# Kernel optimization log

Hardware: AMD Instinct MI355X
Metric: run time of the kernel (lower is better)

The kernel has to match this reference:

```python
import math
import jax, jax.numpy as jnp
import numpy as np

B, T, C = 2, 2048, 1024
N_HEAD = 16
HEAD_DIM = C // N_HEAD

def setup_inputs() -> dict:
    key = jax.random.key(0)
    kx, kq, kk, kv, kp = jax.random.split(key, 5)
    s = 1.0 / math.sqrt(C)
    return {
        "x": jax.random.normal(kx, (B, T, C), dtype=jnp.float32),
        "Wq": jax.random.normal(kq, (C, C), dtype=jnp.float32) * s,
        "Wk": jax.random.normal(kk, (C, C), dtype=jnp.float32) * s,
        "Wv": jax.random.normal(kv, (C, C), dtype=jnp.float32) * s,
        "Wproj": jax.random.normal(kp, (C, C), dtype=jnp.float32) * s,
    }

def reference(x, Wq, Wk, Wv, Wproj):
    b, t, c = x.shape
    # nn.Linear(no bias): x @ W.T ; weights stored [out, in]
    def heads(w):
        return (x @ w.T).reshape(b, t, N_HEAD, HEAD_DIM).transpose(0, 2, 1, 3)  # [B,H,T,D]
    q, k, v = heads(Wq), heads(Wk), heads(Wv)
    att = jnp.einsum('bhqd,bhkd->bhqk', q, k) / math.sqrt(HEAD_DIM)  # [B,H,T,T]
    causal = jnp.tril(jnp.ones((t, t), dtype=bool))
    att = jnp.where(causal, att, -jnp.inf)
    att = jax.nn.softmax(att, axis=-1)
    y = jnp.einsum('bhqk,bhkd->bhqd', att, v)           # [B,H,T,D]
    y = y.transpose(0, 2, 1, 3).reshape(b, t, c)        # [B,T,C]
    return y @ Wproj.T
```

## Files before the change

kernel.cpp:

```cpp
#include <hip/hip_runtime.h>
#include <stdint.h>

typedef uint16_t u16;
typedef uint32_t u32;
typedef __attribute__((ext_vector_type(8))) _Float16 f16x8;
typedef __attribute__((ext_vector_type(4))) float f32x4;

#define NB 2
#define NT 2048
#define NC 1024
#define NH 16
#define ND 64
#define NM (NB*NT)
#define LOG2E 1.44269504088896340736f

__device__ __forceinline__ u16 f2h(float f) {
  _Float16 h = (_Float16)f;
  return __builtin_bit_cast(u16, h);
}

__global__ __launch_bounds__(256) void cvt_kernel(const float* __restrict__ src,
                                                  u16* __restrict__ dst, int n4) {
  int i = blockIdx.x * 256 + threadIdx.x;
  if (i >= n4) return;
  float4 v = ((const float4*)src)[i];
  ushort4 o;
  o.x = f2h(v.x); o.y = f2h(v.y); o.z = f2h(v.z); o.w = f2h(v.w);
  ((ushort4*)dst)[i] = o;
}

__global__ __launch_bounds__(256) void cvtw_kernel(const float* __restrict__ w0,
                                                   const float* __restrict__ w1,
                                                   const float* __restrict__ w2,
                                                   const float* __restrict__ w3,
                                                   u16* __restrict__ dst) {
  int i = blockIdx.x * 256 + threadIdx.x;
  int which = i >> 18;
  const float* src = (which == 0) ? w0 : (which == 1) ? w1 : (which == 2) ? w2 : w3;
  int j = i & 262143;
  float4 v = ((const float4*)src)[j];
  ushort4 o;
  o.x = f2h(v.x); o.y = f2h(v.y); o.z = f2h(v.z); o.w = f2h(v.w);
  ((ushort4*)dst)[i] = o;
}

__device__ __forceinline__ void gload16(const void* g, void* l) {
  __builtin_amdgcn_global_load_lds(
      (const __attribute__((address_space(1))) void*)g,
      (__attribute__((address_space(3))) void*)l, 16, 0, 0);
}

template<int EPI>
__global__ __launch_bounds__(256) void gemm_bt(const u16* __restrict__ A,
                                               const u16* __restrict__ Bw,
                                               int K, int N,
                                               u16* __restrict__ oq, u16* __restrict__ okk,
                                               u16* __restrict__ ovt,
                                               float* __restrict__ of) {
  __shared__ __align__(16) u16 SH[4*128*64];
  u16* Al = SH;
  u16* Bl = SH + 2*128*64;
  const int tid = threadIdx.x, lane = tid & 63, wid = tid >> 6;
  const int g = lane >> 4, qq = lane & 15;
  const int wm = wid >> 1, wn = wid & 1;
  const int m0 = blockIdx.y * 128, n0 = blockIdx.x * 128;
  const int srow = lane >> 3;
  const int scol8 = (lane & 7) ^ srow;

  f32x4 acc[4][4] = {};
  const int nk = K >> 6;

  #pragma unroll
  for (int pp = 0; pp < 4; ++pp) {
    int r = wid*32 + pp*8;
    gload16(A  + (size_t)(m0 + r + srow)*K + scol8*8, &Al[r*64]);
    gload16(Bw + (size_t)(n0 + r + srow)*K + scol8*8, &Bl[r*64]);
  }

  for (int kt = 0; kt < nk; ++kt) {
    const int cur = kt & 1;
    __syncthreads();
    if (kt + 1 < nk) {
      const int k1 = (kt + 1) << 6;
      #pragma unroll
      for (int pp = 0; pp < 4; ++pp) {
        int r = wid*32 + pp*8;
        gload16(A  + (size_t)(m0 + r + srow)*K + k1 + scol8*8, &Al[(cur^1)*8192 + r*64]);
        gload16(Bw + (size_t)(n0 + r + srow)*K + k1 + scol8*8, &Bl[(cur^1)*8192 + r*64]);
      }
    }
    #pragma unroll
    for (int kk = 0; kk < 2; ++kk) {
      f16x8 af[4], bfr[4];
      #pragma unroll
      for (int mt = 0; mt < 4; ++mt) {
        int row = wm*64 + mt*16 + qq;
        af[mt] = *(const f16x8*)&Al[cur*8192 + row*64 + (((kk*4 + g) ^ (qq & 7))*8)];
      }
      #pragma unroll
      for (int nt = 0; nt < 4; ++nt) {
        int row = wn*64 + nt*16 + qq;
        bfr[nt] = *(const f16x8*)&Bl[cur*8192 + row*64 + (((kk*4 + g) ^ (qq & 7))*8)];
      }
      #pragma unroll
      for (int mt = 0; mt < 4; ++mt)
        #pragma unroll
        for (int nt = 0; nt < 4; ++nt)
          acc[mt][nt] = __builtin_amdgcn_mfma_f32_16x16x32_f16(af[mt], bfr[nt], acc[mt][nt], 0, 0, 0);
    }
  }

  if (EPI == 0) {
    __syncthreads();
    u16* reg = SH + wid*4096;
    const int sel = n0 >> 10;
    const int h = ((n0 & 1023) >> 6) + wn;
    const int bq = m0 >> 11;

    if (sel < 2) {
      const float scale = (sel == 0) ? 0.125f*LOG2E : 1.0f;
      #pragma unroll
      for (int mt = 0; mt < 4; ++mt)
        #pragma unroll
        for (int r = 0; r < 4; ++r) {
          int mloc = mt*16 + g*4 + r;
          #pragma unroll
          for (int nt = 0; nt < 4; ++nt) {
            int d = nt*16 + qq;
            reg[mloc*64 + (d ^ (g << 4))] = f2h(acc[mt][nt][r] * scale);
          }
        }
      u16* dst = (sel == 0) ? oq : okk;
      const int slot = lane & 7;
      #pragma unroll
      for (int i = 0; i < 8; ++i) {
        int row = i*8 + (lane >> 3);
        int physslot = slot ^ (((row >> 2) & 3) << 1);
        f16x8 vvv = *(const f16x8*)&reg[row*64 + physslot*8];
        int m = m0 + wm*64 + row;
        int t = m & (NT-1);
        *(f16x8*)(dst + (((size_t)(bq*NH + h)*NT + t)*ND) + slot*8) = vvv;
      }
    } else {
      #pragma unroll
      for (int nt = 0; nt < 4; ++nt) {
        int d = nt*16 + qq;
        int f = (d & 7) << 3;
        #pragma unroll
        for (int mt = 0; mt < 4; ++mt)
          #pragma unroll
          for (int rp = 0; rp < 2; ++rp) {
            int r = rp*2;
            int mloc = mt*16 + g*4 + r;
            u32 pk = (u32)f2h(acc[mt][nt][r]) | ((u32)f2h(acc[mt][nt][r+1]) << 16);
            *(u32*)&reg[d*64 + (mloc ^ f)] = pk;
          }
      }
      const int slot = lane & 7;
      const int t0 = m0 + wm*64;
      #pragma unroll
      for (int i = 0; i < 8; ++i) {
        int d = i*8 + (lane >> 3);
        int physslot = slot ^ (d & 7);
        f16x8 vvv = *(const f16x8*)&reg[d*64 + physslot*8];
        int t = (t0 & (NT-1)) + slot*8;
        *(f16x8*)(ovt + ((size_t)(bq*NH + h)*ND + d)*NT + t) = vvv;
      }
    }
  } else {
    #pragma unroll
    for (int mt = 0; mt < 4; ++mt)
      #pragma unroll
      for (int r = 0; r < 4; ++r) {
        int m = m0 + wm*64 + mt*16 + g*4 + r;
        #pragma unroll
        for (int nt = 0; nt < 4; ++nt) {
          int n = n0 + wn*64 + nt*16 + qq;
          of[(size_t)m*N + n] = acc[mt][nt][r];
        }
      }
  }
}

__global__ __launch_bounds__(256) void attn_kernel(const u16* __restrict__ q,
                                                   const u16* __restrict__ k,
                                                   const u16* __restrict__ vt,
                                                   u16* __restrict__ y) {
  __shared__ __align__(16) u16 Kl[2][64*64];
  __shared__ __align__(16) u16 Vl[2][64*64];
  __shared__ __align__(16) u16 Pl[4*16*64];
  const int tid = threadIdx.x, lane = tid & 63, wid = tid >> 6;
  const int g = lane >> 4, qq = lane & 15;
  const int bh = blockIdx.x;
  const int yy = blockIdx.y;
  const int hmap4[4] = {0, 31, 8, 23};
  const int qtile = yy ^ hmap4[yy >> 3];
  const int qs = qtile * 64;
  const u16* qp = q  + (size_t)bh*NT*ND;
  const u16* kp = k  + (size_t)bh*NT*ND;
  const u16* vp = vt + (size_t)bh*ND*NT;
  const int b = bh >> 4, h = bh & 15;
  const int srow = lane >> 3;
  const int scol8 = (lane & 7) ^ (srow & 7);
  u16* pl = &Pl[wid*1024];
  u32* plw = (u32*)pl;

  f16x8 aq[2];
  {
    int t = qs + wid*16 + qq;
    #pragma unroll
    for (int c = 0; c < 2; ++c)
      aq[c] = *(const f16x8*)(qp + (size_t)t*ND + c*32 + 8*g);
  }

  f16x8 vones;
  #pragma unroll
  for (int i = 0; i < 8; ++i) vones[i] = (_Float16)1.0f;

  f32x4 accO[4] = {};
  f32x4 accS = {};
  float m_run = -1e30f;

  const int ntiles = qtile + 1;

  #pragma unroll
  for (int pp = 0; pp < 2; ++pp) {
    int issue = wid*2 + pp;
    int row = issue*8 + srow;
    gload16(kp + (size_t)row*ND + scol8*8, &Kl[0][issue*512]);
    gload16(vp + (size_t)row*NT + scol8*8, &Vl[0][issue*512]);
  }

  for (int kt = 0; kt < ntiles; ++kt) {
    const int kvs = kt*64;
    const int cur = kt & 1;
    __syncthreads();

    if (kt + 1 < ntiles) {
      const int kvs2 = kvs + 64;
      #pragma unroll
      for (int pp = 0; pp < 2; ++pp) {
        int issue = wid*2 + pp;
        int row = issue*8 + srow;
        gload16(kp + (size_t)(kvs2 + row)*ND + scol8*8, &Kl[cur^1][issue*512]);
        gload16(vp + (size_t)row*NT + kvs2 + scol8*8, &Vl[cur^1][issue*512]);
      }
    }

    f32x4 sacc[4] = {};
    __builtin_amdgcn_s_setprio(1);
    #pragma unroll
    for (int c = 0; c < 2; ++c) {
      #pragma unroll
      for (int nt = 0; nt < 4; ++nt) {
        int row = nt*16 + qq;
        int col = (c*32 + 8*g) ^ ((row & 7) << 3);
        f16x8 kb = *(const f16x8*)&Kl[cur][row*64 + col];
        sacc[nt] = __builtin_amdgcn_mfma_f32_16x16x32_f16(kb, aq[c], sacc[nt], 0, 0, 0);
      }
    }
    __builtin_amdgcn_s_setprio(0);

    if (kvs + 63 > qs + wid*16) {
      int qg = qs + wid*16 + qq;
      #pragma unroll
      for (int nt = 0; nt < 4; ++nt)
        #pragma unroll
        for (int r = 0; r < 4; ++r)
          if (kvs + nt*16 + g*4 + r > qg) sacc[nt][r] = -1e30f;
    }

    float m0a = fmaxf(fmaxf(sacc[0][0], sacc[0][1]), fmaxf(sacc[0][2], sacc[0][3]));
    float m1a = fmaxf(fmaxf(sacc[1][0], sacc[1][1]), fmaxf(sacc[1][2], sacc[1][3]));
    float m2a = fmaxf(fmaxf(sacc[2][0], sacc[2][1]), fmaxf(sacc[2][2], sacc[2][3]));
    float m3a = fmaxf(fmaxf(sacc[3][0], sacc[3][1]), fmaxf(sacc[3][2], sacc[3][3]));
    float mloc = fmaxf(fmaxf(m0a, m1a), fmaxf(m2a, m3a));

    const bool defer = __all(mloc <= m_run + 8.f);
    float mnew;
    if (defer) {
      mnew = m_run;
    } else {
      float mf = fmaxf(mloc, __shfl_xor(mloc, 16));
      mf = fmaxf(mf, __shfl_xor(mf, 32));
      mnew = fmaxf(m_run, mf);
      float a = exp2f(m_run - mnew);
      m_run = mnew;
      #pragma unroll
      for (int r = 0; r < 4; ++r) {
        float ar = __shfl(a, (lane & 48) + g*4 + r);
        #pragma unroll
        for (int nt = 0; nt < 4; ++nt) accO[nt][r] *= ar;
        accS[r] *= ar;
      }
    }

    #pragma unroll
    for (int nt = 0; nt < 4; ++nt) {
      float p0 = exp2f(sacc[nt][0] - mnew);
      float p1 = exp2f(sacc[nt][1] - mnew);
      float p2 = exp2f(sacc[nt][2] - mnew);
      float p3 = exp2f(sacc[nt][3] - mnew);
      u32 pk0 = __builtin_bit_cast(u32, __builtin_amdgcn_cvt_pkrtz(p0, p1));
      u32 pk1 = __builtin_bit_cast(u32, __builtin_amdgcn_cvt_pkrtz(p2, p3));
      int kv0 = nt*16 + g*4;
      plw[(qq*64 + (kv0 ^ ((qq & 7) << 3))) >> 1] = pk0;
      plw[(qq*64 + ((kv0 + 2) ^ ((qq & 7) << 3))) >> 1] = pk1;
    }

    __builtin_amdgcn_s_setprio(1);
    #pragma unroll
    for (int c = 0; c < 2; ++c) {
      f16x8 pa = *(const f16x8*)&pl[qq*64 + ((c*32 + 8*g) ^ ((qq & 7) << 3))];
      accS = __builtin_amdgcn_mfma_f32_16x16x32_f16(pa, vones, accS, 0, 0, 0);
      #pragma unroll
      for (int nt = 0; nt < 4; ++nt) {
        int vrow = nt*16 + qq;
        int vcol = (c*32 + 8*g) ^ ((vrow & 7) << 3);
        f16x8 vb = *(const f16x8*)&Vl[cur][vrow*64 + vcol];
        accO[nt] = __builtin_amdgcn_mfma_f32_16x16x32_f16(pa, vb, accO[nt], 0, 0, 0);
      }
    }
    __builtin_amdgcn_s_setprio(0);
  }

  #pragma unroll
  for (int r = 0; r < 4; ++r) {
    float invr = 1.0f / accS[r];
    int t = qs + wid*16 + g*4 + r;
    #pragma unroll
    for (int nt = 0; nt < 4; ++nt) {
      int d = nt*16 + qq;
      y[((size_t)(b*NT + t))*NC + h*ND + d] = f2h(accO[nt][r] * invr);
    }
  }
}

extern "C" void kernel_launch(void* const* d_in, const int* in_sizes, int n_in,
                              void* d_out, int out_size, void* d_ws, size_t ws_size,
                              hipStream_t stream) {
  const float* x  = (const float*)d_in[0];
  const float* Wq = (const float*)d_in[1];
  const float* Wk = (const float*)d_in[2];
  const float* Wv = (const float*)d_in[3];
  const float* Wp = (const float*)d_in[4];

  u16* xb   = (u16*)d_ws;
  u16* wqkv = xb   + (size_t)NM*NC;
  u16* wpj  = wqkv + (size_t)3*NC*NC;
  u16* qb   = wpj  + (size_t)NC*NC;
  u16* kb   = qb   + (size_t)NM*NC;
  u16* vtb  = kb   + (size_t)NM*NC;
  u16* yb   = vtb  + (size_t)NM*NC;
  size_t need = ((size_t)NM*NC*5 + (size_t)4*NC*NC) * sizeof(u16);
  if (ws_size < need) return;

  cvt_kernel<<<NM*NC/4/256, 256, 0, stream>>>(x, xb, NM*NC/4);
  cvtw_kernel<<<4*NC*NC/4/256, 256, 0, stream>>>(Wq, Wk, Wv, Wp, wqkv);

  gemm_bt<0><<<dim3(3*NC/128, NM/128), 256, 0, stream>>>(xb, wqkv, NC, 3*NC,
                                                         qb, kb, vtb, nullptr);
  attn_kernel<<<dim3(NB*NH, 32), 256, 0, stream>>>(qb, kb, vtb, yb);
  gemm_bt<1><<<dim3(NC/128, NM/128), 256, 0, stream>>>(yb, wpj, NC, NC,
                                                       nullptr, nullptr, nullptr,
                                                       (float*)d_out);
}
```

Baseline: 115.8 us.

## Split long causal query tiles into two KV chunks with a combine pass

Each of the 16 longest query tiles per head now has its KV range split into two chunks, which run as separate blocks. Every block takes its query tile, KV start, chunk count and mode from a static work table ordered longest first. Split blocks write normalized partial outputs plus row max and sum to a scratch area that reuses the x buffer, and a new combine kernel merges them with log-sum-exp weights. The aim is to even out the causal load imbalance and shorten the critical path, at the cost of an extra launch, scratch traffic and partials stored in fp16. The P store to LDS is also widened to one 64-bit write.

```diff
diff --git a/kernel.cpp b/kernel.cpp
--- a/kernel.cpp
+++ b/kernel.cpp
@@ -5,6 +5,7 @@
 typedef uint32_t u32;
 typedef __attribute__((ext_vector_type(8))) _Float16 f16x8;
 typedef __attribute__((ext_vector_type(4))) float f32x4;
+typedef __attribute__((ext_vector_type(2))) uint32_t u32x2;
 
 #define NB 2
 #define NT 2048
@@ -13,6 +14,7 @@
 #define ND 64
 #define NM (NB*NT)
 #define LOG2E 1.44269504088896340736f
+#define PSTRIDE 4608
 
 __device__ __forceinline__ u16 f2h(float f) {
   _Float16 h = (_Float16)f;
@@ -182,19 +184,36 @@
   }
 }
 
+#define IT(q,s,c,m) ((u32)(q) | ((u32)(s)<<8) | ((u32)(c)<<16) | ((u32)(m)<<24))
 __global__ __launch_bounds__(256) void attn_kernel(const u16* __restrict__ q,
                                                    const u16* __restrict__ k,
                                                    const u16* __restrict__ vt,
-                                                   u16* __restrict__ y) {
+                                                   u16* __restrict__ y,
+                                                   u16* __restrict__ part) {
+  static const u32 items[48] = {
+    IT(15,0,16,0), IT(30,0,16,1), IT(31,0,16,1), IT(31,16,16,2),
+    IT(14,0,15,0), IT(28,0,15,1), IT(29,0,15,1), IT(29,15,15,2), IT(30,16,15,2),
+    IT(13,0,14,0), IT(26,0,14,1), IT(27,0,14,1), IT(27,14,14,2), IT(28,15,14,2),
+    IT(12,0,13,0), IT(24,0,13,1), IT(25,0,13,1), IT(25,13,13,2), IT(26,14,13,2),
+    IT(11,0,12,0), IT(22,0,12,1), IT(23,0,12,1), IT(23,12,12,2), IT(24,13,12,2),
+    IT(10,0,11,0), IT(20,0,11,1), IT(21,0,11,1), IT(21,11,11,2), IT(22,12,11,2),
+    IT( 9,0,10,0), IT(18,0,10,1), IT(19,0,10,1), IT(19,10,10,2), IT(20,11,10,2),
+    IT( 8,0, 9,0), IT(16,0, 9,1), IT(17,0, 9,1), IT(17, 9, 9,2), IT(18,10, 9,2),
+    IT( 7,0, 8,0), IT(16,9, 8,2),
+    IT( 6,0, 7,0), IT( 5,0, 6,0), IT( 4,0, 5,0), IT( 3,0, 4,0),
+    IT( 2,0, 3,0), IT( 1,0, 2,0), IT( 0,0, 1,0)
+  };
   __shared__ __align__(16) u16 Kl[2][64*64];
   __shared__ __align__(16) u16 Vl[2][64*64];
   __shared__ __align__(16) u16 Pl[4*16*64];
   const int tid = threadIdx.x, lane = tid & 63, wid = tid >> 6;
   const int g = lane >> 4, qq = lane & 15;
   const int bh = blockIdx.x;
-  const int yy = blockIdx.y;
-  const int hmap4[4] = {0, 31, 8, 23};
-  const int qtile = yy ^ hmap4[yy >> 3];
+  const u32 it = items[blockIdx.y];
+  const int qtile = it & 255;
+  const int ks = (it >> 8) & 255;
+  const int kc = (it >> 16) & 255;
+  const int mode = it >> 24;
   const int qs = qtile * 64;
   const u16* qp = q  + (size_t)bh*NT*ND;
   const u16* kp = k  + (size_t)bh*NT*ND;
@@ -221,22 +240,20 @@
   f32x4 accS = {};
   float m_run = -1e30f;
 
-  const int ntiles = qtile + 1;
-
   #pragma unroll
   for (int pp = 0; pp < 2; ++pp) {
     int issue = wid*2 + pp;
     int row = issue*8 + srow;
-    gload16(kp + (size_t)row*ND + scol8*8, &Kl[0][issue*512]);
-    gload16(vp + (size_t)row*NT + scol8*8, &Vl[0][issue*512]);
-  }
-
-  for (int kt = 0; kt < ntiles; ++kt) {
+    gload16(kp + (size_t)(ks*64 + row)*ND + scol8*8, &Kl[0][issue*512]);
+    gload16(vp + (size_t)row*NT + ks*64 + scol8*8, &Vl[0][issue*512]);
+  }
+
+  for (int kt = ks; kt < ks + kc; ++kt) {
     const int kvs = kt*64;
-    const int cur = kt & 1;
+    const int cur = (kt - ks) & 1;
     __syncthreads();
 
-    if (kt + 1 < ntiles) {
+    if (kt + 1 < ks + kc) {
       const int kvs2 = kvs + 64;
       #pragma unroll
       for (int pp = 0; pp < 2; ++pp) {
@@ -304,8 +321,8 @@
       u32 pk0 = __builtin_bit_cast(u32, __builtin_amdgcn_cvt_pkrtz(p0, p1));
       u32 pk1 = __builtin_bit_cast(u32, __builtin_amdgcn_cvt_pkrtz(p2, p3));
       int kv0 = nt*16 + g*4;
-      plw[(qq*64 + (kv0 ^ ((qq & 7) << 3))) >> 1] = pk0;
-      plw[(qq*64 + ((kv0 + 2) ^ ((qq & 7) << 3))) >> 1] = pk1;
+      u32x2 pr; pr.x = pk0; pr.y = pk1;
+      *(u32x2*)&plw[(qq*64 + (kv0 ^ ((qq & 7) << 3))) >> 1] = pr;
     }
 
     __builtin_amdgcn_s_setprio(1);
@@ -324,15 +341,65 @@
     __builtin_amdgcn_s_setprio(0);
   }
 
+  if (mode == 0) {
+    #pragma unroll
+    for (int r = 0; r < 4; ++r) {
+      float invr = 1.0f / accS[r];
+      int t = qs + wid*16 + g*4 + r;
+      #pragma unroll
+      for (int nt = 0; nt < 4; ++nt) {
+        int d = nt*16 + qq;
+        y[((size_t)(b*NT + t))*NC + h*ND + d] = f2h(accO[nt][r] * invr);
+      }
+    }
+  } else {
+    const int slot = ((bh << 4) + (qtile - 16))*2 + (mode - 1);
+    u16* pp = part + (size_t)slot * PSTRIDE;
+    float* hd = (float*)(pp + 4096);
+    #pragma unroll
+    for (int r = 0; r < 4; ++r) {
+      int rloc = wid*16 + g*4 + r;
+      float l = accS[r];
+      float invr = 1.0f / l;
+      float mr = __shfl(m_run, (lane & 48) + g*4 + r);
+      #pragma unroll
+      for (int nt = 0; nt < 4; ++nt) {
+        int d = nt*16 + qq;
+        pp[rloc*64 + d] = f2h(accO[nt][r] * invr);
+      }
+      if (qq == 0) { hd[rloc] = mr; hd[64 + rloc] = l; }
+    }
+  }
+}
+
+__global__ __launch_bounds__(256) void combine_kernel(const u16* __restrict__ part,
+                                                      u16* __restrict__ y) {
+  const int jj = blockIdx.x;
+  const int bh = blockIdx.y;
+  const int b = bh >> 4, h = bh & 15;
+  const u16* p0 = part + (size_t)(((bh << 4) + jj)*2) * PSTRIDE;
+  const u16* p1 = p0 + PSTRIDE;
+  const float* h0 = (const float*)(p0 + 4096);
+  const float* h1 = (const float*)(p1 + 4096);
+  const int tid = threadIdx.x;
+  const int d0 = (tid & 7) * 8;
   #pragma unroll
-  for (int r = 0; r < 4; ++r) {
-    float invr = 1.0f / accS[r];
-    int t = qs + wid*16 + g*4 + r;
-    #pragma unroll
-    for (int nt = 0; nt < 4; ++nt) {
-      int d = nt*16 + qq;
-      y[((size_t)(b*NT + t))*NC + h*ND + d] = f2h(accO[nt][r] * invr);
-    }
+  for (int i = 0; i < 2; ++i) {
+    int r = (tid >> 3) + 32*i;
+    float m1 = h0[r], l1 = h0[64 + r];
+    float m2 = h1[r], l2 = h1[64 + r];
+    float mm = fmaxf(m1, m2);
+    float w1 = exp2f(m1 - mm) * l1, w2 = exp2f(m2 - mm) * l2;
+    float inv = 1.0f / (w1 + w2);
+    float a1 = w1 * inv, a2 = w2 * inv;
+    f16x8 o1 = *(const f16x8*)&p0[r*64 + d0];
+    f16x8 o2 = *(const f16x8*)&p1[r*64 + d0];
+    f16x8 out;
+    #pragma unroll
+    for (int e = 0; e < 8; ++e)
+      out[e] = (_Float16)(a1 * (float)o1[e] + a2 * (float)o2[e]);
+    int t = (16 + jj)*64 + r;
+    *(f16x8*)(y + ((size_t)(b*NT + t))*NC + h*ND + d0) = out;
   }
 }
 
@@ -352,6 +419,7 @@
   u16* kb   = qb   + (size_t)NM*NC;
   u16* vtb  = kb   + (size_t)NM*NC;
   u16* yb   = vtb  + (size_t)NM*NC;
+  u16* part = xb;
   size_t need = ((size_t)NM*NC*5 + (size_t)4*NC*NC) * sizeof(u16);
   if (ws_size < need) return;
 
@@ -360,7 +428,8 @@
 
   gemm_bt<0><<<dim3(3*NC/128, NM/128), 256, 0, stream>>>(xb, wqkv, NC, 3*NC,
                                                          qb, kb, vtb, nullptr);
-  attn_kernel<<<dim3(NB*NH, 32), 256, 0, stream>>>(qb, kb, vtb, yb);
+  attn_kernel<<<dim3(NB*NH, 48), 256, 0, stream>>>(qb, kb, vtb, yb, part);
+  combine_kernel<<<dim3(16, NB*NH), 256, 0, stream>>>(part, yb);
   gemm_bt<1><<<dim3(NC/128, NM/128), 256, 0, stream>>>(yb, wpj, NC, NC,
                                                        nullptr, nullptr, nullptr,
                                                        (float*)d_out);
```

Result: faster. 113.0 us (-2.4%).
